# Kernel optimization log

Hardware: AMD Instinct MI355X
Metric: run time of the kernel (lower is better)

The kernel has to match this reference:

```python
import jax, jax.numpy as jnp
import numpy as np

X_SIZE = 1024
N_HEADS = 16
N_BASIS = 10
MAX_LEN = 4096
CACHE_KEEP_LEN = 4096
B = 8
T_NEW = 128
T_PREV = 4096
HEAD_DIM = X_SIZE // N_HEADS
LN_EPS = 1e-5


def setup_inputs() -> dict:
    key = jax.random.key(0)
    ks = jax.random.split(key, 9)
    def w(k, shape, s):
        return jax.random.normal(k, shape, dtype=jnp.float32) * s
    inv = 1.0 / np.sqrt(X_SIZE)
    return {
        "X": w(ks[0], (B, T_NEW, X_SIZE), 1.0),
        "cache_K": w(ks[1], (B, T_PREV, X_SIZE), 1.0),
        "cache_V": w(ks[2], (B, T_PREV, X_SIZE), 1.0),
        "Wq": w(ks[3], (X_SIZE, X_SIZE), 0.1 * inv),   # Q_SCALE=0.1 (NormedLinear init scale)
        "bq": jnp.zeros((X_SIZE,), jnp.float32),
        "Wk": w(ks[4], (X_SIZE, X_SIZE), 0.2 * inv),   # K_SCALE=0.2, no bias
        "Wv": w(ks[5], (X_SIZE, X_SIZE), 1.0 * inv),   # V_SCALE*sqrt(scale), no bias
        "Wproj": w(ks[6], (X_SIZE, X_SIZE), 1.0 * inv),
        "bproj": jnp.zeros((X_SIZE,), jnp.float32),
        "Wr": w(ks[7], (X_SIZE, N_BASIS * N_HEADS), 0.1 * inv),  # R_SCALE=0.1
        "br": jnp.zeros((N_BASIS * N_HEADS,), jnp.float32),
        "b_nd": w(ks[8], (N_BASIS, MAX_LEN), 0.2),     # B_SCALE=0.2
        "ln_g": jnp.ones((X_SIZE,), jnp.float32),
        "ln_b": jnp.zeros((X_SIZE,), jnp.float32),
    }


def _split_heads(x, h):
    b, t, e = x.shape
    return x.reshape(b, t, h, e // h).transpose(0, 2, 1, 3).reshape(b * h, t, e // h)


def _merge_heads(x, h):
    bh, t, q = x.shape
    b = bh // h
    return x.reshape(b, h, t, q).transpose(0, 2, 1, 3).reshape(b, t, h * q)


def reference(X, cache_K, cache_V, Wq, bq, Wk, Wv, Wproj, bproj, Wr, br, b_nd, ln_g, ln_b):
    Bsz, t, E = X.shape
    # ln_x
    mu = jnp.mean(X, axis=-1, keepdims=True)
    var = jnp.var(X, axis=-1, keepdims=True)
    Xn = (X - mu) / jnp.sqrt(var + LN_EPS) * ln_g + ln_b
    # projections on new tokens
    Q = Xn @ Wq + bq
    K_new = Xn @ Wk
    V_new = Xn @ Wv
    # update_state: append cache (startfull=max(Tprev-cache_keep_len,0))
    Tprev = cache_K.shape[1]
    start = max(Tprev - CACHE_KEEP_LEN, 0)
    Kf = jnp.concatenate([cache_K[:, start:], K_new], axis=1)  # (B, T, E)
    Vf = jnp.concatenate([cache_V[:, start:], V_new], axis=1)
    T = Kf.shape[1]
    Qh = _split_heads(Q, N_HEADS)   # (B*h, t, q)
    Kh = _split_heads(Kf, N_HEADS)  # (B*h, T, q)
    Vh = _split_heads(Vf, N_HEADS)
    # relattn logits: R_btn (B*h, t, n_basis), bandified basis D_ntT
    R = _split_heads(Xn @ Wr + br, N_HEADS)
    d = (T - t + jnp.arange(t)[:, None]) - jnp.arange(T)[None, :]  # (t, T) time diff
    valid = (d >= 0) & (d < MAX_LEN)
    D = jnp.where(valid[None, :, :], b_nd[:, jnp.clip(d, 0, MAX_LEN - 1)], 0.0)  # (n, t, T)
    extra = jnp.einsum('btn,ntT->btT', R, D)  # (B*h, t, T)
    # causal band bias (mask=None -> default causal mask with maxlen window)
    bias = jnp.where(valid, 0.0, -1e9)[None, :, :]
    logits = bias + extra + jnp.einsum('btq,bTq->btT', Qh, Kh) * (1.0 / np.sqrt(HEAD_DIM))
    W_btT = jax.nn.softmax(logits, axis=-1)
    A = _merge_heads(jnp.einsum('btT,bTq->btq', W_btT, Vh), N_HEADS)  # (B, t, E)
    return X + (A @ Wproj + bproj)
```

## Files before the change

### kernel.cpp

```cpp
#include <hip/hip_runtime.h>
#include <hip/hip_bf16.h>

typedef __bf16 bf16;
typedef __bf16 bf16x8 __attribute__((ext_vector_type(8)));
typedef float f32x4 __attribute__((ext_vector_type(4)));
typedef unsigned short u16;
typedef u16 u16x4 __attribute__((ext_vector_type(4)));

#define MFMA16(a, b, c) __builtin_amdgcn_mfma_f32_16x16x32_bf16(a, b, c, 0, 0, 0)
#define LOG2E 1.44269504f

static __device__ __forceinline__ bf16x8 cvt8(float4 a, float4 b) {
  union { bf16 h[8]; bf16x8 v; } u;
  u.h[0] = (bf16)a.x; u.h[1] = (bf16)a.y; u.h[2] = (bf16)a.z; u.h[3] = (bf16)a.w;
  u.h[4] = (bf16)b.x; u.h[5] = (bf16)b.y; u.h[6] = (bf16)b.z; u.h[7] = (bf16)b.w;
  return u.v;
}

__global__ __launch_bounds__(256) void k_ln(const float* __restrict__ X,
                                            const float* __restrict__ g,
                                            const float* __restrict__ bb,
                                            bf16* __restrict__ Xn) {
  int m = blockIdx.x, t = threadIdx.x;
  const float* row = X + (size_t)m * 1024;
  float4 x = ((const float4*)row)[t];
  float s1 = x.x + x.y + x.z + x.w;
  float s2 = x.x * x.x + x.y * x.y + x.z * x.z + x.w * x.w;
#pragma unroll
  for (int off = 1; off < 64; off <<= 1) {
    s1 += __shfl_xor(s1, off);
    s2 += __shfl_xor(s2, off);
  }
  __shared__ float ws1[4], ws2[4];
  int w = t >> 6;
  if ((t & 63) == 0) { ws1[w] = s1; ws2[w] = s2; }
  __syncthreads();
  s1 = ws1[0] + ws1[1] + ws1[2] + ws1[3];
  s2 = ws2[0] + ws2[1] + ws2[2] + ws2[3];
  float mu = s1 * (1.f / 1024.f);
  float var = s2 * (1.f / 1024.f) - mu * mu;
  float rstd = rsqrtf(var + 1e-5f);
  float4 gg = ((const float4*)g)[t];
  float4 bv = ((const float4*)bb)[t];
  union { bf16 h[4]; u16x4 v; } u;
  u.h[0] = (bf16)((x.x - mu) * rstd * gg.x + bv.x);
  u.h[1] = (bf16)((x.y - mu) * rstd * gg.y + bv.y);
  u.h[2] = (bf16)((x.z - mu) * rstd * gg.z + bv.z);
  u.h[3] = (bf16)((x.w - mu) * rstd * gg.w + bv.w);
  ((u16x4*)(Xn + (size_t)m * 1024))[t] = u.v;
}

__global__ __launch_bounds__(256) void k_convert(const float* __restrict__ Wq,
                                                 const float* __restrict__ Wk,
                                                 const float* __restrict__ Wv,
                                                 const float* __restrict__ Wr,
                                                 const float* __restrict__ Wp,
                                                 bf16* __restrict__ Wt_all,
                                                 bf16* __restrict__ Wpt) {
  __shared__ float tile[64][65];
  int t = threadIdx.x;
  int bn = blockIdx.x / 16, bk = blockIdx.x % 16;
  int n0 = bn * 64, k0 = bk * 64;
#pragma unroll
  for (int it = 0; it < 16; ++it) {
    int idx = t + 256 * it;
    int kl = idx >> 6, nl = idx & 63;
    int n = n0 + nl, k = k0 + kl;
    float v;
    if (n < 1024)       v = Wq[(size_t)k * 1024 + n];
    else if (n < 2048)  v = Wk[(size_t)k * 1024 + (n - 1024)];
    else if (n < 3072)  v = Wv[(size_t)k * 1024 + (n - 2048)];
    else if (n < 3232)  v = Wr[(size_t)k * 160 + (n - 3072)];
    else if (n < 3328)  v = 0.f;
    else                v = Wp[(size_t)k * 1024 + (n - 3328)];
    tile[kl][nl] = v;
  }
  __syncthreads();
#pragma unroll
  for (int it = 0; it < 16; ++it) {
    int idx = t + 256 * it;
    int nl = idx >> 6, kl = idx & 63;
    int n = n0 + nl, k = k0 + kl;
    bf16 v = (bf16)tile[kl][nl];
    if (n < 3328) Wt_all[(size_t)n * 1024 + k] = v;
    else          Wpt[(size_t)(n - 3328) * 1024 + k] = v;
  }
}

template <int MODE>
__global__ __launch_bounds__(256) void k_gemm(const bf16* __restrict__ A,
                                              const bf16* __restrict__ Bw,
                                              bf16* __restrict__ Qb, bf16* __restrict__ Kn,
                                              bf16* __restrict__ Vn, float* __restrict__ Rws,
                                              const float* __restrict__ bq,
                                              const float* __restrict__ br,
                                              float* __restrict__ Out,
                                              const float* __restrict__ bproj,
                                              const float* __restrict__ Xres) {
  __shared__ __align__(16) bf16 As[128][72];
  __shared__ __align__(16) bf16 Bs[128][72];
  int t = threadIdx.x, l = t & 63, wid = t >> 6;
  int ln = l & 15, grp = l >> 4;
  int m0 = blockIdx.y * 128, n0 = blockIdx.x * 128;
  int wr = wid >> 1, wc = wid & 1;
  f32x4 acc[4][4] = {};
  int srow = t >> 1, shalf = (t & 1) * 32;

  for (int kt = 0; kt < 16; ++kt) {
    int k0 = kt * 64;
    const bf16* asrc = A + (size_t)(m0 + srow) * 1024 + k0 + shalf;
    const bf16* bsrc = Bw + (size_t)(n0 + srow) * 1024 + k0 + shalf;
    bf16x8 a0 = ((const bf16x8*)asrc)[0], a1 = ((const bf16x8*)asrc)[1];
    bf16x8 a2 = ((const bf16x8*)asrc)[2], a3 = ((const bf16x8*)asrc)[3];
    bf16x8 b0 = ((const bf16x8*)bsrc)[0], b1 = ((const bf16x8*)bsrc)[1];
    bf16x8 b2 = ((const bf16x8*)bsrc)[2], b3 = ((const bf16x8*)bsrc)[3];
    __syncthreads();
    *(bf16x8*)&As[srow][shalf + 0] = a0;  *(bf16x8*)&As[srow][shalf + 8] = a1;
    *(bf16x8*)&As[srow][shalf + 16] = a2; *(bf16x8*)&As[srow][shalf + 24] = a3;
    *(bf16x8*)&Bs[srow][shalf + 0] = b0;  *(bf16x8*)&Bs[srow][shalf + 8] = b1;
    *(bf16x8*)&Bs[srow][shalf + 16] = b2; *(bf16x8*)&Bs[srow][shalf + 24] = b3;
    __syncthreads();
#pragma unroll
    for (int ks = 0; ks < 2; ++ks) {
      int kk = ks * 32 + grp * 8;
      bf16x8 af[4], bf[4];
#pragma unroll
      for (int is = 0; is < 4; ++is) af[is] = *(const bf16x8*)&As[wr * 64 + is * 16 + ln][kk];
#pragma unroll
      for (int js = 0; js < 4; ++js) bf[js] = *(const bf16x8*)&Bs[wc * 64 + js * 16 + ln][kk];
#pragma unroll
      for (int is = 0; is < 4; ++is)
#pragma unroll
        for (int js = 0; js < 4; ++js) acc[is][js] = MFMA16(af[is], bf[js], acc[is][js]);
    }
  }

#pragma unroll
  for (int is = 0; is < 4; ++is)
#pragma unroll
    for (int js = 0; js < 4; ++js)
#pragma unroll
      for (int r = 0; r < 4; ++r) {
        int m = m0 + wr * 64 + is * 16 + grp * 4 + r;
        int n = n0 + wc * 64 + js * 16 + ln;
        float v = acc[is][js][r];
        if (MODE == 0) {
          int b = m >> 7, il = m & 127;
          if (n < 1024) {
            int h = n >> 6, dm = n & 63;
            Qb[((size_t)(b * 16 + h) * 128 + il) * 64 + dm] = (bf16)((v + bq[n]) * (0.125f * LOG2E));
          } else if (n < 2048) {
            Kn[(size_t)m * 1024 + (n - 1024)] = (bf16)v;
          } else if (n < 3072) {
            Vn[(size_t)m * 1024 + (n - 2048)] = (bf16)v;
          } else if (n < 3232) {
            int e = n - 3072, hh = e / 10, nb = e - hh * 10;
            Rws[((size_t)(b * 16 + hh) * 128 + il) * 10 + nb] = v + br[e];
          }
        } else {
          Out[(size_t)m * 1024 + n] = v + bproj[n] + Xres[(size_t)m * 1024 + n];
        }
      }
}

__global__ __launch_bounds__(512, 4) void k_attn(const float* __restrict__ cacheK,
                                                 const float* __restrict__ cacheV,
                                                 const bf16* __restrict__ Kn,
                                                 const bf16* __restrict__ Vn,
                                                 const bf16* __restrict__ Qb,
                                                 const float* __restrict__ Rws,
                                                 const float* __restrict__ bnd,
                                                 bf16* __restrict__ Opart,
                                                 float* __restrict__ mws,
                                                 float* __restrict__ lws) {
  __shared__ __align__(16) bf16 Ks[2][64][72];
  __shared__ __align__(16) bf16 Vt[2][64][72];
  __shared__ __align__(16) bf16 Gw[8][80][20];
  __shared__ __align__(16) bf16 bTf[516][16];

  int t = threadIdx.x, l = t & 63, w = t >> 6;
  int grp = l >> 4, ln = l & 15;
  int s = blockIdx.x % 12, bh = blockIdx.x / 12;
  int b = bh >> 4, h = bh & 15;
  int toff = s < 6 ? s * 6 : 36 + (s - 6) * 5;
  int nt   = s < 6 ? 6 : 5;
  int jbase = toff * 64;
  int dlo0 = 4033 - jbase;

  {
    int q = t;
    int d = dlo0 - 320 + q;
    d = d < 0 ? 0 : (d > 4095 ? 4095 : d);
#pragma unroll
    for (int n = 0; n < 10; ++n) bTf[q][n] = (bf16)bnd[(size_t)n * 4096 + d];
#pragma unroll
    for (int n = 10; n < 16; ++n) bTf[q][n] = (bf16)0.f;
  }
  if (t < 4) {
#pragma unroll
    for (int n = 0; n < 16; ++n) bTf[512 + t][n] = (bf16)0.f;
  }

  int iq = w * 16 + ln;
  bf16x8 qf[2];
  qf[0] = *(const bf16x8*)(Qb + ((size_t)bh * 128 + iq) * 64 + grp * 8);
  qf[1] = *(const bf16x8*)(Qb + ((size_t)bh * 128 + iq) * 64 + 32 + grp * 8);
  bf16x8 rf;
  {
    union { bf16 hh[8]; bf16x8 v; } u;
    const float* rrow = Rws + ((size_t)bh * 128 + iq) * 10;
#pragma unroll
    for (int e = 0; e < 8; ++e) {
      int k = grp * 8 + e;
      u.hh[e] = (bf16)(k < 10 ? rrow[k] * LOG2E : 0.f);
    }
    rf = u.v;
  }

  int krow = t >> 3, kcb = (t & 7) * 8;
  int vjl = t & 63, vd0 = (t >> 6) * 8;
  int vsp = (((vjl & 3) >> 1) << 5) | (((vjl >> 2) & 3) << 3) | ((vjl >> 4) << 1) | (vjl & 1);

  float4 kA, kB, vA, vB;

  auto issue = [&](int jt0) {
    if (jt0 < 4096) {
      const float* src = cacheK + ((size_t)(b * 4096 + jt0 + krow)) * 1024 + h * 64 + kcb;
      kA = *(const float4*)src;
      kB = *(const float4*)(src + 4);
      const float* sv = cacheV + ((size_t)(b * 4096 + jt0 + vjl)) * 1024 + h * 64 + vd0;
      vA = *(const float4*)sv;
      vB = *(const float4*)(sv + 4);
    } else {
      bf16x8 kN = *(const bf16x8*)(Kn + ((size_t)(b * 128 + (jt0 + krow - 4096))) * 1024 + h * 64 + kcb);
      bf16x8 vN = *(const bf16x8*)(Vn + ((size_t)(b * 128 + (jt0 + vjl - 4096))) * 1024 + h * 64 + vd0);
      kA = make_float4((float)kN[0], (float)kN[1], (float)kN[2], (float)kN[3]);
      kB = make_float4((float)kN[4], (float)kN[5], (float)kN[6], (float)kN[7]);
      vA = make_float4((float)vN[0], (float)vN[1], (float)vN[2], (float)vN[3]);
      vB = make_float4((float)vN[4], (float)vN[5], (float)vN[6], (float)vN[7]);
    }
  };
  auto stage = [&](int p) {
    *(bf16x8*)&Ks[p][krow][kcb] = cvt8(kA, kB);
    Vt[p][vd0 + 0][vsp] = (bf16)vA.x; Vt[p][vd0 + 1][vsp] = (bf16)vA.y;
    Vt[p][vd0 + 2][vsp] = (bf16)vA.z; Vt[p][vd0 + 3][vsp] = (bf16)vA.w;
    Vt[p][vd0 + 4][vsp] = (bf16)vB.x; Vt[p][vd0 + 5][vsp] = (bf16)vB.y;
    Vt[p][vd0 + 6][vsp] = (bf16)vB.z; Vt[p][vd0 + 7][vsp] = (bf16)vB.w;
  };

  issue(jbase);
  stage(0);
  issue(jbase + 64);

  f32x4 Oacc[4] = {};
  float m_r = -1e30f, l_r = 0.f;

  for (int tt = 0; tt < nt; ++tt) {
    int jt0 = jbase + tt * 64;
    int cur = tt & 1;
    __syncthreads();
    if (tt + 1 < nt) stage(cur ^ 1);
    if (tt + 2 < nt) issue(jbase + (tt + 2) * 64);

    __builtin_amdgcn_s_setprio(1);
    f32x4 Sacc[4] = {};
#pragma unroll
    for (int ks = 0; ks < 2; ++ks) {
      int kk = ks * 32 + grp * 8;
#pragma unroll
      for (int js = 0; js < 4; ++js) {
        bf16x8 bfr = *(const bf16x8*)&Ks[cur][js * 16 + ln][kk];
        Sacc[js] = MFMA16(bfr, qf[ks], Sacc[js]);
      }
    }
    int qb = 320 - 64 * tt;
#pragma unroll
    for (int u = 0; u < 5; ++u) {
      bf16x8 bfr = *(const bf16x8*)&bTf[qb + (w + u) * 16 + ln][grp * 8];
      f32x4 z = {};
      f32x4 g = MFMA16(rf, bfr, z);
      union { bf16 hh[4]; u16x4 v; } uu;
      uu.hh[0] = (bf16)g[0]; uu.hh[1] = (bf16)g[1];
      uu.hh[2] = (bf16)g[2]; uu.hh[3] = (bf16)g[3];
      *(u16x4*)&Gw[w][u * 16 + ln][grp * 4] = uu.v;
    }
    __builtin_amdgcn_s_setprio(0);

    float mx = -1e30f;
    if (jt0 >= 128 && jt0 < 4034) {
#pragma unroll
      for (int js = 0; js < 4; ++js)
#pragma unroll
        for (int r = 0; r < 4; ++r) {
          int jj = js * 16 + grp * 4 + r;
          int cl = 63 + ln - jj;
          float v = Sacc[js][r] + (float)Gw[w][cl][ln];
          Sacc[js][r] = v;
          mx = fmaxf(mx, v);
        }
    } else {
#pragma unroll
      for (int js = 0; js < 4; ++js)
#pragma unroll
        for (int r = 0; r < 4; ++r) {
          int jj = js * 16 + grp * 4 + r;
          int d = 4096 + iq - (jt0 + jj);
          bool valid = ((unsigned)d) < 4096u;
          int cl = 63 + ln - jj;
          float g = (float)Gw[w][cl][ln];
          float v = valid ? (Sacc[js][r] + g) : -1e9f;
          Sacc[js][r] = v;
          mx = fmaxf(mx, v);
        }
    }
    mx = fmaxf(mx, __shfl_xor(mx, 16));
    mx = fmaxf(mx, __shfl_xor(mx, 32));
    float mnew = fmaxf(m_r, mx);
    float scn = exp2f(m_r - mnew);
    m_r = mnew;

    union { bf16 hh[8]; bf16x8 v; } p0, p1;
    float rsl = 0.f;
#pragma unroll
    for (int js = 0; js < 4; ++js)
#pragma unroll
      for (int r = 0; r < 4; ++r) {
        float p = exp2f(Sacc[js][r] - mnew);
        rsl += p;
        if (r < 2) p0.hh[js * 2 + r] = (bf16)p;
        else       p1.hh[js * 2 + (r - 2)] = (bf16)p;
      }
    l_r = l_r * scn + rsl;

#pragma unroll
    for (int r = 0; r < 4; ++r) {
      float scr = __shfl(scn, grp * 4 + r, 16);
#pragma unroll
      for (int ds = 0; ds < 4; ++ds) Oacc[ds][r] *= scr;
    }

    __builtin_amdgcn_s_setprio(1);
#pragma unroll
    for (int ds = 0; ds < 4; ++ds) {
      bf16x8 v0 = *(const bf16x8*)&Vt[cur][ds * 16 + ln][grp * 8];
      bf16x8 v1 = *(const bf16x8*)&Vt[cur][ds * 16 + ln][32 + grp * 8];
      Oacc[ds] = MFMA16(p0.v, v0, Oacc[ds]);
      Oacc[ds] = MFMA16(p1.v, v1, Oacc[ds]);
    }
    __builtin_amdgcn_s_setprio(0);
  }

  l_r += __shfl_xor(l_r, 16);
  l_r += __shfl_xor(l_r, 32);

  int part = s * 128 + bh;
#pragma unroll
  for (int ds = 0; ds < 4; ++ds)
#pragma unroll
    for (int r = 0; r < 4; ++r) {
      int il = w * 16 + grp * 4 + r;
      Opart[((size_t)part * 128 + il) * 64 + ds * 16 + ln] = (bf16)Oacc[ds][r];
    }
  if (grp == 0) {
    mws[(size_t)part * 128 + iq] = m_r;
    lws[(size_t)part * 128 + iq] = l_r;
  }
}

__global__ __launch_bounds__(256) void k_combine(const bf16* __restrict__ Opart,
                                                 const float* __restrict__ mws,
                                                 const float* __restrict__ lws,
                                                 bf16* __restrict__ Aout) {
  __shared__ float msh[12][32], lsh[12][32];
  int bh = blockIdx.x, q = blockIdx.y, t = threadIdx.x;
  int b = bh >> 4, h = bh & 15;
  for (int idx = t; idx < 384; idx += 256) {
    int s = idx >> 5, io = idx & 31;
    msh[s][io] = mws[(size_t)(s * 128 + bh) * 128 + q * 32 + io];
    lsh[s][io] = lws[(size_t)(s * 128 + bh) * 128 + q * 32 + io];
  }
  __syncthreads();
  int dm = t & 63, i4 = t >> 6;
  for (int ii = 0; ii < 8; ++ii) {
    int io = i4 * 8 + ii;
    int i = q * 32 + io;
    float M = -1e30f;
#pragma unroll
    for (int s = 0; s < 12; ++s) M = fmaxf(M, msh[s][io]);
    float L = 0.f, acc = 0.f;
#pragma unroll
    for (int s = 0; s < 12; ++s) {
      float wgt = exp2f(msh[s][io] - M);
      L += wgt * lsh[s][io];
      acc += wgt * (float)Opart[((size_t)(s * 128 + bh) * 128 + i) * 64 + dm];
    }
    Aout[((size_t)(b * 128 + i)) * 1024 + h * 64 + dm] = (bf16)(acc / L);
  }
}

extern "C" void kernel_launch(void* const* d_in, const int* in_sizes, int n_in,
                              void* d_out, int out_size, void* d_ws, size_t ws_size,
                              hipStream_t stream) {
  (void)in_sizes; (void)n_in; (void)out_size; (void)ws_size;
  const float* X      = (const float*)d_in[0];
  const float* cacheK = (const float*)d_in[1];
  const float* cacheV = (const float*)d_in[2];
  const float* Wq     = (const float*)d_in[3];
  const float* bq     = (const float*)d_in[4];
  const float* Wk     = (const float*)d_in[5];
  const float* Wv     = (const float*)d_in[6];
  const float* Wproj  = (const float*)d_in[7];
  const float* bproj  = (const float*)d_in[8];
  const float* Wr     = (const float*)d_in[9];
  const float* br     = (const float*)d_in[10];
  const float* bnd    = (const float*)d_in[11];
  const float* lng    = (const float*)d_in[12];
  const float* lnb    = (const float*)d_in[13];
  float* out = (float*)d_out;

  char* ws = (char*)d_ws;
  bf16* Wt_all = (bf16*)ws;  ws += (size_t)3328 * 1024 * 2;
  bf16* Wpt    = (bf16*)ws;  ws += (size_t)1024 * 1024 * 2;
  bf16* Xn     = (bf16*)ws;  ws += (size_t)1024 * 1024 * 2;
  bf16* Qb     = (bf16*)ws;  ws += (size_t)1024 * 1024 * 2;
  bf16* Kn     = (bf16*)ws;  ws += (size_t)1024 * 1024 * 2;
  bf16* Vn     = (bf16*)ws;  ws += (size_t)1024 * 1024 * 2;
  bf16* Aattn  = (bf16*)ws;  ws += (size_t)1024 * 1024 * 2;
  float* Rws   = (float*)ws; ws += (size_t)128 * 128 * 10 * 4;
  float* mws   = (float*)ws; ws += (size_t)12 * 128 * 128 * 4;
  float* lws   = (float*)ws; ws += (size_t)12 * 128 * 128 * 4;
  bf16* Opart  = (bf16*)ws;  ws += (size_t)12 * 128 * 128 * 64 * 2;

  k_convert<<<dim3(68 * 16), 256, 0, stream>>>(Wq, Wk, Wv, Wr, Wproj, Wt_all, Wpt);
  k_ln<<<dim3(1024), 256, 0, stream>>>(X, lng, lnb, Xn);
  k_gemm<0><<<dim3(26, 8), 256, 0, stream>>>(Xn, Wt_all, Qb, Kn, Vn, Rws, bq, br,
                                             nullptr, nullptr, nullptr);
  k_attn<<<dim3(1536), 512, 0, stream>>>(cacheK, cacheV, Kn, Vn, Qb, Rws, bnd,
                                         Opart, mws, lws);
  k_combine<<<dim3(128, 4), 256, 0, stream>>>(Opart, mws, lws, Aattn);
  k_gemm<1><<<dim3(8, 8), 256, 0, stream>>>(Aattn, Wpt, nullptr, nullptr, nullptr,
                                            nullptr, nullptr, nullptr, out, bproj, X);
}
```

Before: 175.8 us.

## Halve attention KV tile to 32 keys and add lazy softmax rescaling

```diff
diff --git a/kernel.cpp b/kernel.cpp
--- a/kernel.cpp
+++ b/kernel.cpp
@@ -173,18 +173,16 @@
                                                  bf16* __restrict__ Opart,
                                                  float* __restrict__ mws,
                                                  float* __restrict__ lws) {
-  __shared__ __align__(16) bf16 Ks[2][64][72];
-  __shared__ __align__(16) bf16 Vt[2][64][72];
-  __shared__ __align__(16) bf16 Gw[8][80][20];
+  __shared__ __align__(16) bf16 Ks[2][32][72];
+  __shared__ __align__(16) bf16 Vt[2][64][36];
+  __shared__ __align__(16) bf16 Gw[8][48][20];
   __shared__ __align__(16) bf16 bTf[516][16];
 
   int t = threadIdx.x, l = t & 63, w = t >> 6;
   int grp = l >> 4, ln = l & 15;
   int s = blockIdx.x % 12, bh = blockIdx.x / 12;
   int b = bh >> 4, h = bh & 15;
-  int toff = s < 6 ? s * 6 : 36 + (s - 6) * 5;
-  int nt   = s < 6 ? 6 : 5;
-  int jbase = toff * 64;
+  int jbase = s * 352;
   int dlo0 = 4033 - jbase;
 
   {
@@ -217,66 +215,64 @@
     rf = u.v;
   }
 
-  int krow = t >> 3, kcb = (t & 7) * 8;
-  int vjl = t & 63, vd0 = (t >> 6) * 8;
-  int vsp = (((vjl & 3) >> 1) << 5) | (((vjl >> 2) & 3) << 3) | ((vjl >> 4) << 1) | (vjl & 1);
-
-  float4 kA, kB, vA, vB;
+  int krow = t >> 4, kcb = (t & 15) * 4;
+  int vjl = t & 31, vd0 = (t >> 5) * 4;
+  int vsp = (((vjl >> 2) & 3) << 3) | (((vjl >> 4) & 1) << 2) | (vjl & 3);
+
+  float4 kA, vA;
 
   auto issue = [&](int jt0) {
     if (jt0 < 4096) {
-      const float* src = cacheK + ((size_t)(b * 4096 + jt0 + krow)) * 1024 + h * 64 + kcb;
-      kA = *(const float4*)src;
-      kB = *(const float4*)(src + 4);
-      const float* sv = cacheV + ((size_t)(b * 4096 + jt0 + vjl)) * 1024 + h * 64 + vd0;
-      vA = *(const float4*)sv;
-      vB = *(const float4*)(sv + 4);
+      kA = *(const float4*)(cacheK + ((size_t)(b * 4096 + jt0 + krow)) * 1024 + h * 64 + kcb);
+      vA = *(const float4*)(cacheV + ((size_t)(b * 4096 + jt0 + vjl)) * 1024 + h * 64 + vd0);
     } else {
-      bf16x8 kN = *(const bf16x8*)(Kn + ((size_t)(b * 128 + (jt0 + krow - 4096))) * 1024 + h * 64 + kcb);
-      bf16x8 vN = *(const bf16x8*)(Vn + ((size_t)(b * 128 + (jt0 + vjl - 4096))) * 1024 + h * 64 + vd0);
-      kA = make_float4((float)kN[0], (float)kN[1], (float)kN[2], (float)kN[3]);
-      kB = make_float4((float)kN[4], (float)kN[5], (float)kN[6], (float)kN[7]);
-      vA = make_float4((float)vN[0], (float)vN[1], (float)vN[2], (float)vN[3]);
-      vB = make_float4((float)vN[4], (float)vN[5], (float)vN[6], (float)vN[7]);
+      u16x4 kN = *(const u16x4*)(Kn + ((size_t)(b * 128 + (jt0 + krow - 4096))) * 1024 + h * 64 + kcb);
+      u16x4 vN = *(const u16x4*)(Vn + ((size_t)(b * 128 + (jt0 + vjl - 4096))) * 1024 + h * 64 + vd0);
+      union { u16 u; bf16 h; } c;
+      c.u = kN[0]; kA.x = (float)c.h; c.u = kN[1]; kA.y = (float)c.h;
+      c.u = kN[2]; kA.z = (float)c.h; c.u = kN[3]; kA.w = (float)c.h;
+      c.u = vN[0]; vA.x = (float)c.h; c.u = vN[1]; vA.y = (float)c.h;
+      c.u = vN[2]; vA.z = (float)c.h; c.u = vN[3]; vA.w = (float)c.h;
     }
   };
   auto stage = [&](int p) {
-    *(bf16x8*)&Ks[p][krow][kcb] = cvt8(kA, kB);
+    union { bf16 hh[4]; u16x4 v; } ku;
+    ku.hh[0] = (bf16)kA.x; ku.hh[1] = (bf16)kA.y;
+    ku.hh[2] = (bf16)kA.z; ku.hh[3] = (bf16)kA.w;
+    *(u16x4*)&Ks[p][krow][kcb] = ku.v;
     Vt[p][vd0 + 0][vsp] = (bf16)vA.x; Vt[p][vd0 + 1][vsp] = (bf16)vA.y;
     Vt[p][vd0 + 2][vsp] = (bf16)vA.z; Vt[p][vd0 + 3][vsp] = (bf16)vA.w;
-    Vt[p][vd0 + 4][vsp] = (bf16)vB.x; Vt[p][vd0 + 5][vsp] = (bf16)vB.y;
-    Vt[p][vd0 + 6][vsp] = (bf16)vB.z; Vt[p][vd0 + 7][vsp] = (bf16)vB.w;
   };
 
   issue(jbase);
   stage(0);
-  issue(jbase + 64);
+  issue(jbase + 32);
 
   f32x4 Oacc[4] = {};
   float m_r = -1e30f, l_r = 0.f;
 
-  for (int tt = 0; tt < nt; ++tt) {
-    int jt0 = jbase + tt * 64;
+  for (int tt = 0; tt < 11; ++tt) {
+    int jt0 = jbase + tt * 32;
     int cur = tt & 1;
     __syncthreads();
-    if (tt + 1 < nt) stage(cur ^ 1);
-    if (tt + 2 < nt) issue(jbase + (tt + 2) * 64);
+    if (tt + 1 < 11) stage(cur ^ 1);
+    if (tt + 2 < 11) issue(jbase + (tt + 2) * 32);
 
     __builtin_amdgcn_s_setprio(1);
-    f32x4 Sacc[4] = {};
+    f32x4 Sacc[2] = {};
 #pragma unroll
     for (int ks = 0; ks < 2; ++ks) {
       int kk = ks * 32 + grp * 8;
 #pragma unroll
-      for (int js = 0; js < 4; ++js) {
+      for (int js = 0; js < 2; ++js) {
         bf16x8 bfr = *(const bf16x8*)&Ks[cur][js * 16 + ln][kk];
         Sacc[js] = MFMA16(bfr, qf[ks], Sacc[js]);
       }
     }
-    int qb = 320 - 64 * tt;
-#pragma unroll
-    for (int u = 0; u < 5; ++u) {
-      bf16x8 bfr = *(const bf16x8*)&bTf[qb + (w + u) * 16 + ln][grp * 8];
+    int qb = 352 - 32 * tt;
+#pragma unroll
+    for (int u = 0; u < 3; ++u) {
+      bf16x8 bfr = *(const bf16x8*)&bTf[qb + w * 16 + u * 16 + ln][grp * 8];
       f32x4 z = {};
       f32x4 g = MFMA16(rf, bfr, z);
       union { bf16 hh[4]; u16x4 v; } uu;
@@ -287,26 +283,26 @@
     __builtin_amdgcn_s_setprio(0);
 
     float mx = -1e30f;
-    if (jt0 >= 128 && jt0 < 4034) {
-#pragma unroll
-      for (int js = 0; js < 4; ++js)
+    if (jt0 >= 128 && jt0 < 4066) {
+#pragma unroll
+      for (int js = 0; js < 2; ++js)
 #pragma unroll
         for (int r = 0; r < 4; ++r) {
           int jj = js * 16 + grp * 4 + r;
-          int cl = 63 + ln - jj;
+          int cl = ln - jj + 31;
           float v = Sacc[js][r] + (float)Gw[w][cl][ln];
           Sacc[js][r] = v;
           mx = fmaxf(mx, v);
         }
     } else {
 #pragma unroll
-      for (int js = 0; js < 4; ++js)
+      for (int js = 0; js < 2; ++js)
 #pragma unroll
         for (int r = 0; r < 4; ++r) {
           int jj = js * 16 + grp * 4 + r;
           int d = 4096 + iq - (jt0 + jj);
           bool valid = ((unsigned)d) < 4096u;
-          int cl = 63 + ln - jj;
+          int cl = ln - jj + 31;
           float g = (float)Gw[w][cl][ln];
           float v = valid ? (Sacc[js][r] + g) : -1e9f;
           Sacc[js][r] = v;
@@ -315,37 +311,37 @@
     }
     mx = fmaxf(mx, __shfl_xor(mx, 16));
     mx = fmaxf(mx, __shfl_xor(mx, 32));
-    float mnew = fmaxf(m_r, mx);
-    float scn = exp2f(m_r - mnew);
-    m_r = mnew;
-
-    union { bf16 hh[8]; bf16x8 v; } p0, p1;
+
+    if (!__all(mx <= m_r + 8.f)) {
+      float mnew = fmaxf(m_r, mx);
+      float scn = exp2f(m_r - mnew);
+      m_r = mnew;
+      l_r *= scn;
+#pragma unroll
+      for (int r = 0; r < 4; ++r) {
+        float scr = __shfl(scn, grp * 4 + r, 16);
+#pragma unroll
+        for (int ds = 0; ds < 4; ++ds) Oacc[ds][r] *= scr;
+      }
+    }
+
+    union { bf16 hh[8]; bf16x8 v; } p0;
     float rsl = 0.f;
 #pragma unroll
-    for (int js = 0; js < 4; ++js)
+    for (int js = 0; js < 2; ++js)
 #pragma unroll
       for (int r = 0; r < 4; ++r) {
-        float p = exp2f(Sacc[js][r] - mnew);
+        float p = exp2f(Sacc[js][r] - m_r);
         rsl += p;
-        if (r < 2) p0.hh[js * 2 + r] = (bf16)p;
-        else       p1.hh[js * 2 + (r - 2)] = (bf16)p;
+        p0.hh[js * 4 + r] = (bf16)p;
       }
-    l_r = l_r * scn + rsl;
-
-#pragma unroll
-    for (int r = 0; r < 4; ++r) {
-      float scr = __shfl(scn, grp * 4 + r, 16);
-#pragma unroll
-      for (int ds = 0; ds < 4; ++ds) Oacc[ds][r] *= scr;
-    }
+    l_r += rsl;
 
     __builtin_amdgcn_s_setprio(1);
 #pragma unroll
     for (int ds = 0; ds < 4; ++ds) {
       bf16x8 v0 = *(const bf16x8*)&Vt[cur][ds * 16 + ln][grp * 8];
-      bf16x8 v1 = *(const bf16x8*)&Vt[cur][ds * 16 + ln][32 + grp * 8];
       Oacc[ds] = MFMA16(p0.v, v0, Oacc[ds]);
-      Oacc[ds] = MFMA16(p1.v, v1, Oacc[ds]);
     }
     __builtin_amdgcn_s_setprio(0);
   }
```

Result: faster. 163.1 us (-7.2%).
